# Optimization experiments

Measured on AMD Instinct MI355X. Metric: run time of the kernel, lower is better.

## Reference

```python
import jax, jax.numpy as jnp
import numpy as np

EMBED = 1024
HEADS = 16
HEAD_DIM = EMBED // HEADS
NEG = -1e20


def setup_inputs() -> dict:
    key = jax.random.key(0)
    k1, k2, k3, k4, k5, k6 = jax.random.split(key, 6)
    N, S = 2, 2048
    values = jax.random.normal(k1, (N, S, EMBED), dtype=jnp.float32)
    keys = jax.random.normal(k2, (N, S, EMBED), dtype=jnp.float32)
    query = jax.random.normal(k3, (N, S, EMBED), dtype=jnp.float32)
    mask = jax.random.randint(k4, (N, 1, S, S), 0, 2, dtype=jnp.int32)
    # fc_out: Linear(embed, embed) with bias; torch layout W [out, in]
    W_fc = jax.random.normal(k5, (EMBED, EMBED), dtype=jnp.float32) * (1.0 / np.sqrt(EMBED))
    b_fc = jax.random.normal(k6, (EMBED,), dtype=jnp.float32) * 0.01
    return {"values": values, "keys": keys, "query": query, "mask": mask,
            "W_fc": W_fc, "b_fc": b_fc}


def reference(values, keys, query, mask, W_fc, b_fc):
    N, Q, E = query.shape
    K = keys.shape[1]
    H, D = HEADS, HEAD_DIM
    v = values.reshape(N, K, H, D)
    k = keys.reshape(N, K, H, D)
    q = query.reshape(N, Q, H, D)
    # energy: [N, H, Q, K]
    energy = jnp.einsum('nqhd,nkhd->nhqk', q, k)
    energy = jnp.where(mask == 0, NEG, energy)
    # NOTE: original scales by sqrt(embed_size), not sqrt(head_dim)
    attn = jax.nn.softmax(energy / jnp.sqrt(jnp.float32(E)), axis=3)
    out = jnp.einsum('nhqk,nkhd->nqhd', attn, v).reshape(N, Q, H * D)
    return out @ W_fc.T + b_fc
```

## Files before the change

kernel.cpp:

```cpp
#include <hip/hip_runtime.h>
#include <cmath>

#define S_LEN 2048
#define EMB   1024
#define NHEAD 16
#define DHEAD 64
#define PIT   72

typedef __attribute__((ext_vector_type(8))) short bf16x8;
typedef __attribute__((ext_vector_type(4))) float f32x4;

__device__ __forceinline__ unsigned short f2bf(float f){
    union { float f; unsigned u; } v; v.f = f;
    unsigned r = v.u + 0x7fffu + ((v.u >> 16) & 1u);
    return (unsigned short)(r >> 16);
}

__device__ __forceinline__ unsigned pk2bf(float a, float b){
#if __has_builtin(__builtin_amdgcn_cvt_pk_bf16_f32)
    typedef __attribute__((ext_vector_type(2))) __bf16 bf2;
    bf2 r = __builtin_amdgcn_cvt_pk_bf16_f32(a, b);
    return *(unsigned*)&r;
#else
    return (unsigned)f2bf(a) | ((unsigned)f2bf(b) << 16);
#endif
}

__device__ __forceinline__ float fast_exp2(float x){
#if __has_builtin(__builtin_amdgcn_exp2f)
    return __builtin_amdgcn_exp2f(x);
#else
    return exp2f(x);
#endif
}

__device__ __forceinline__ float fast_rcp(float x){
#if __has_builtin(__builtin_amdgcn_rcpf)
    return __builtin_amdgcn_rcpf(x);
#else
    return 1.0f / x;
#endif
}

__global__ void prep_all(const float* __restrict__ q, const float* __restrict__ k,
                         const float* __restrict__ v, const int* __restrict__ mask,
                         const float* __restrict__ W,
                         unsigned short* __restrict__ Qb, unsigned short* __restrict__ Kb,
                         unsigned short* __restrict__ Vt, unsigned short* __restrict__ Wb,
                         unsigned* __restrict__ Mb){
    __shared__ unsigned short tile[64*68];
    const int b = blockIdx.x, tid = threadIdx.x;
    if (b < 4096){
        const float SC = 0.045084220027780106f;
        int base = (b*256 + tid) * 4;
        int e = base & (EMB - 1);
        int s = (base >> 10) & (S_LEN - 1);
        int n = base >> 21;
        int h = e >> 6, d = e & 63;
        int dst = ((n*NHEAD + h)*S_LEN + s)*DHEAD + d;
        float4 qv = *(const float4*)(q + base);
        float4 kv = *(const float4*)(k + base);
        uint2 qp, kp;
        qp.x = pk2bf(qv.x*SC, qv.y*SC);
        qp.y = pk2bf(qv.z*SC, qv.w*SC);
        kp.x = pk2bf(kv.x, kv.y);
        kp.y = pk2bf(kv.z, kv.w);
        *(uint2*)(Qb + dst) = qp;
        *(uint2*)(Kb + dst) = kp;
    } else if (b < 5120){
        int idx = b - 4096;
        int st = idx & 31, h = (idx >> 5) & 15, n = idx >> 9;
        int sbase = st * 64;
#pragma unroll
        for (int i = 0; i < 4; i++){
            int c = tid + i*256;
            int srow = c >> 4, c4 = (c & 15) * 4;
            float4 x = *(const float4*)(v + (n*S_LEN + sbase + srow)*EMB + h*DHEAD + c4);
            uint2 p;
            p.x = pk2bf(x.x, x.y);
            p.y = pk2bf(x.z, x.w);
            *(uint2*)&tile[srow*68 + c4] = p;
        }
        __syncthreads();
#pragma unroll
        for (int i = 0; i < 2; i++){
            int c = tid + i*256;
            int d = c >> 3, s8 = (c & 7) * 8;
            unsigned u0 = (unsigned)tile[(s8+0)*68 + d] | ((unsigned)tile[(s8+1)*68 + d] << 16);
            unsigned u1 = (unsigned)tile[(s8+2)*68 + d] | ((unsigned)tile[(s8+3)*68 + d] << 16);
            unsigned u2 = (unsigned)tile[(s8+4)*68 + d] | ((unsigned)tile[(s8+5)*68 + d] << 16);
            unsigned u3 = (unsigned)tile[(s8+6)*68 + d] | ((unsigned)tile[(s8+7)*68 + d] << 16);
            uint4 pk; pk.x = u0; pk.y = u1; pk.z = u2; pk.w = u3;
            *(uint4*)(Vt + ((n*NHEAD + h)*DHEAD + d)*S_LEN + sbase + s8) = pk;
        }
    } else if (b < 6144){
        int base = ((b - 5120)*256 + tid) * 4;
        float4 x = *(const float4*)(W + base);
        uint2 p;
        p.x = pk2bf(x.x, x.y);
        p.y = pk2bf(x.z, x.w);
        *(uint2*)(Wb + base) = p;
    } else {
        int u = (b - 6144)*256 + tid;
        const int4* m4 = (const int4*)mask + (size_t)u*8;
        unsigned w = 0;
#pragma unroll
        for (int i = 0; i < 8; i++){
            int4 m = m4[i];
            unsigned nib = (m.x ? 1u : 0u) | (m.y ? 2u : 0u) | (m.z ? 4u : 0u) | (m.w ? 8u : 0u);
            w |= nib << (i*4);
        }
        Mb[u] = w;
    }
}

__global__ __launch_bounds__(256, 4) void flash_attn(
    const unsigned short* __restrict__ Qb, const unsigned short* __restrict__ Kb,
    const unsigned short* __restrict__ Vt, const unsigned* __restrict__ Mb,
    float* __restrict__ Op, float* __restrict__ Lp){
    __shared__ unsigned short Kt[64*PIT];
    __shared__ unsigned short Vl[64*PIT];
    __shared__ unsigned short Pt[4][32*PIT];
    __shared__ uint2 mlut[16];

    const int tid = threadIdx.x;
    if (tid < 16){
        uint2 e;
        e.x = ((tid & 1) ? 0xFFFFu : 0u) | ((tid & 2) ? 0xFFFF0000u : 0u);
        e.y = ((tid & 4) ? 0xFFFFu : 0u) | ((tid & 8) ? 0xFFFF0000u : 0u);
        mlut[tid] = e;
    }

    const int flat = blockIdx.x + (blockIdx.y << 4) + (blockIdx.z << 9);
    const int xcd = flat & 7, idx = flat >> 3;
    const int qt = idx & 15;
    const int sl = xcd + ((idx >> 4) << 3);
    const int h = sl & 15, split = (sl >> 4) & 1, n = sl >> 5;

    const int wave = tid >> 6, lane = tid & 63, il = lane & 15, quad = lane >> 4;
    const int qbase = qt*128 + wave*32;
    const int kbase = split*1024;

    const unsigned short* Qh = Qb + (n*NHEAD + h)*S_LEN*DHEAD;
    const unsigned short* Kh = Kb + (n*NHEAD + h)*S_LEN*DHEAD + kbase*DHEAD;
    const unsigned short* Vh = Vt + (n*NHEAD + h)*DHEAD*S_LEN + kbase;
    const unsigned* mr0 = Mb + (size_t)(n*S_LEN + qbase + il)*(S_LEN/32) + (kbase >> 5);
    const unsigned* mr1 = mr0 + 16*(S_LEN/32);
    Op += (size_t)split * (2*S_LEN*EMB);
    Lp += split * (2*NHEAD*S_LEN);

    const int srow = tid >> 3, scol = (tid & 7)*8;

    bf16x8 Qf[2][2];
#pragma unroll
    for (int rt = 0; rt < 2; rt++)
#pragma unroll
        for (int ks = 0; ks < 2; ks++)
            Qf[rt][ks] = *(const bf16x8*)(Qh + (qbase + rt*16 + il)*DHEAD + ks*32 + quad*8);

    f32x4 acc[2][4], accL[2];
#pragma unroll
    for (int rt = 0; rt < 2; rt++){
        accL[rt] = (f32x4){0.f,0.f,0.f,0.f};
#pragma unroll
        for (int j = 0; j < 4; j++) acc[rt][j] = (f32x4){0.f,0.f,0.f,0.f};
    }
    const short onev = 0x3F80;
    const bf16x8 onesb = {onev,onev,onev,onev,onev,onev,onev,onev};

    unsigned short* Pw = Pt[wave];
    const int q4 = quad*4;

    uint4 kpre0 = *(const uint4*)(Kh + srow*DHEAD + scol);
    uint4 kpre1 = *(const uint4*)(Kh + (srow + 32)*DHEAD + scol);
    uint4 vpre0 = *(const uint4*)(Vh + srow*S_LEN + scol);
    uint4 vpre1 = *(const uint4*)(Vh + (srow + 32)*S_LEN + scol);

    for (int kb = 0; kb < 1024; kb += 64){
        *(uint4*)&Kt[srow*PIT + scol]        = kpre0;
        *(uint4*)&Kt[(srow + 32)*PIT + scol] = kpre1;
        *(uint4*)&Vl[srow*PIT + scol]        = vpre0;
        *(uint4*)&Vl[(srow + 32)*PIT + scol] = vpre1;
        __syncthreads();
        uint2 w0 = *(const uint2*)(mr0 + (kb >> 5));
        uint2 w1 = *(const uint2*)(mr1 + (kb >> 5));
        if (kb + 64 < 1024){
            kpre0 = *(const uint4*)(Kh + (kb + 64 + srow)*DHEAD + scol);
            kpre1 = *(const uint4*)(Kh + (kb + 64 + srow + 32)*DHEAD + scol);
            vpre0 = *(const uint4*)(Vh + srow*S_LEN + kb + 64 + scol);
            vpre1 = *(const uint4*)(Vh + (srow + 32)*S_LEN + kb + 64 + scol);
        }

        f32x4 e[2][4];
#pragma unroll
        for (int t = 0; t < 4; t++){
            bf16x8 kf0 = *(const bf16x8*)(&Kt[(t*16 + il)*PIT + quad*8]);
            bf16x8 kf1 = *(const bf16x8*)(&Kt[(t*16 + il)*PIT + 32 + quad*8]);
#pragma unroll
            for (int rt = 0; rt < 2; rt++){
                f32x4 z = (f32x4){0.f,0.f,0.f,0.f};
                z        = __builtin_amdgcn_mfma_f32_16x16x32_bf16(kf0, Qf[rt][0], z, 0, 0, 0);
                e[rt][t] = __builtin_amdgcn_mfma_f32_16x16x32_bf16(kf1, Qf[rt][1], z, 0, 0, 0);
            }
        }
#pragma unroll
        for (int rt = 0; rt < 2; rt++){
            const uint2 w = rt ? w1 : w0;
            unsigned s0 = w.x >> q4, s1 = w.y >> q4;
            unsigned s0h = s0 >> 16, s1h = s1 >> 16;
#pragma unroll
            for (int t = 0; t < 4; t++){
                unsigned s = (t == 0) ? s0 : (t == 1) ? s0h : (t == 2) ? s1 : s1h;
                uint2 mw = mlut[s & 0xFu];
                float p0 = fast_exp2(e[rt][t][0]);
                float p1 = fast_exp2(e[rt][t][1]);
                float p2 = fast_exp2(e[rt][t][2]);
                float p3 = fast_exp2(e[rt][t][3]);
                uint2 pk;
                pk.x = pk2bf(p0, p1) & mw.x;
                pk.y = pk2bf(p2, p3) & mw.y;
                *(uint2*)&Pw[(rt*16 + il)*PIT + t*16 + quad*4] = pk;
            }
        }
#pragma unroll
        for (int kk = 0; kk < 2; kk++){
            bf16x8 Pa[2];
#pragma unroll
            for (int rt = 0; rt < 2; rt++){
                Pa[rt] = *(const bf16x8*)(&Pw[(rt*16 + il)*PIT + kk*32 + quad*8]);
                accL[rt] = __builtin_amdgcn_mfma_f32_16x16x32_bf16(Pa[rt], onesb, accL[rt], 0, 0, 0);
            }
#pragma unroll
            for (int dt = 0; dt < 4; dt++){
                bf16x8 Vf = *(const bf16x8*)(&Vl[(dt*16 + il)*PIT + kk*32 + quad*8]);
#pragma unroll
                for (int rt = 0; rt < 2; rt++)
                    acc[rt][dt] = __builtin_amdgcn_mfma_f32_16x16x32_bf16(Pa[rt], Vf, acc[rt][dt], 0, 0, 0);
            }
        }
        __syncthreads();
    }

#pragma unroll
    for (int rt = 0; rt < 2; rt++){
#pragma unroll
        for (int dt = 0; dt < 4; dt++)
#pragma unroll
            for (int r = 0; r < 4; r++){
                size_t row = (size_t)(n*S_LEN + qbase + rt*16 + quad*4 + r);
                Op[row*EMB + h*DHEAD + dt*16 + il] = acc[rt][dt][r];
            }
        if (il == 0){
#pragma unroll
            for (int r = 0; r < 4; r++)
                Lp[(n*NHEAD + h)*S_LEN + qbase + rt*16 + quad*4 + r] = accL[rt][r];
        }
    }
}

__global__ __launch_bounds__(256, 2) void gemm_norm(
    const float* __restrict__ Op0, const float* __restrict__ Op1,
    const float* __restrict__ Lp0, const float* __restrict__ Lp1,
    const unsigned short* __restrict__ W, const float* __restrict__ bias,
    float* __restrict__ out){
    __shared__ unsigned short At[128*PIT];
    __shared__ unsigned short Wt[64*PIT];
    const int flat = blockIdx.x + (blockIdx.y << 4);
    const int xcd = flat & 7, idx = flat >> 3;
    const int nb = idx & 15, mb = xcd*4 + (idx >> 4);
    const int tid = threadIdx.x;
    const int wave = tid >> 6, lane = tid & 63, il = lane & 15, quad = lane >> 4;
    const int wm = wave & 1, wn = wave >> 1;
    const int mbase = mb*128, nbase = nb*64;
    const int arow = tid >> 3, acol = (tid & 7)*8;
    const int n_blk = mbase >> 11, qoff = (mbase & (S_LEN-1));
    const float* La = Lp0 + n_blk*NHEAD*S_LEN + qoff;
    const float* Lb = Lp1 + n_blk*NHEAD*S_LEN + qoff;

    f32x4 acc[4][2];
#pragma unroll
    for (int i = 0; i < 4; i++)
#pragma unroll
        for (int j = 0; j < 2; j++) acc[i][j] = (f32x4){0.f,0.f,0.f,0.f};

    float4 apre[4][2], bpre[4][2]; float lpa[4], lpb[4]; uint4 wpre[2];
#pragma unroll
    for (int j = 0; j < 4; j++){
        size_t off = (size_t)(mbase + arow + j*32)*EMB + acol;
        apre[j][0] = *(const float4*)(Op0 + off);
        apre[j][1] = *(const float4*)(Op0 + off + 4);
        bpre[j][0] = *(const float4*)(Op1 + off);
        bpre[j][1] = *(const float4*)(Op1 + off + 4);
        lpa[j] = La[arow + j*32];
        lpb[j] = Lb[arow + j*32];
    }
#pragma unroll
    for (int j = 0; j < 2; j++)
        wpre[j] = *(const uint4*)(W + (size_t)(nbase + arow + j*32)*EMB + acol);

    for (int kb = 0; kb < EMB; kb += 64){
#pragma unroll
        for (int j = 0; j < 4; j++){
            float inv = fast_rcp(lpa[j] + lpb[j]);
            uint4 pk;
            pk.x = pk2bf((apre[j][0].x + bpre[j][0].x)*inv, (apre[j][0].y + bpre[j][0].y)*inv);
            pk.y = pk2bf((apre[j][0].z + bpre[j][0].z)*inv, (apre[j][0].w + bpre[j][0].w)*inv);
            pk.z = pk2bf((apre[j][1].x + bpre[j][1].x)*inv, (apre[j][1].y + bpre[j][1].y)*inv);
            pk.w = pk2bf((apre[j][1].z + bpre[j][1].z)*inv, (apre[j][1].w + bpre[j][1].w)*inv);
            *(uint4*)&At[(arow + j*32)*PIT + acol] = pk;
        }
#pragma unroll
        for (int j = 0; j < 2; j++)
            *(uint4*)&Wt[(arow + j*32)*PIT + acol] = wpre[j];
        __syncthreads();
        if (kb + 64 < EMB){
            int h = (kb + 64) >> 6;
#pragma unroll
            for (int j = 0; j < 4; j++){
                size_t off = (size_t)(mbase + arow + j*32)*EMB + kb + 64 + acol;
                apre[j][0] = *(const float4*)(Op0 + off);
                apre[j][1] = *(const float4*)(Op0 + off + 4);
                bpre[j][0] = *(const float4*)(Op1 + off);
                bpre[j][1] = *(const float4*)(Op1 + off + 4);
                lpa[j] = La[h*S_LEN + arow + j*32];
                lpb[j] = Lb[h*S_LEN + arow + j*32];
            }
#pragma unroll
            for (int j = 0; j < 2; j++)
                wpre[j] = *(const uint4*)(W + (size_t)(nbase + arow + j*32)*EMB + kb + 64 + acol);
        }
#pragma unroll
        for (int ks = 0; ks < 2; ks++){
            bf16x8 Af[4], Wf[2];
#pragma unroll
            for (int mt = 0; mt < 4; mt++)
                Af[mt] = *(const bf16x8*)(&At[(wm*64 + mt*16 + il)*PIT + ks*32 + quad*8]);
#pragma unroll
            for (int nt = 0; nt < 2; nt++)
                Wf[nt] = *(const bf16x8*)(&Wt[(wn*32 + nt*16 + il)*PIT + ks*32 + quad*8]);
#pragma unroll
            for (int mt = 0; mt < 4; mt++)
#pragma unroll
                for (int nt = 0; nt < 2; nt++)
                    acc[mt][nt] = __builtin_amdgcn_mfma_f32_16x16x32_bf16(Af[mt], Wf[nt], acc[mt][nt], 0, 0, 0);
        }
        __syncthreads();
    }
    float bb[2];
#pragma unroll
    for (int nt = 0; nt < 2; nt++) bb[nt] = bias[nbase + wn*32 + nt*16 + il];
#pragma unroll
    for (int mt = 0; mt < 4; mt++)
#pragma unroll
        for (int nt = 0; nt < 2; nt++)
#pragma unroll
            for (int r = 0; r < 4; r++){
                int row = mbase + wm*64 + mt*16 + quad*4 + r;
                int col = nbase + wn*32 + nt*16 + il;
                out[(size_t)row*EMB + col] = acc[mt][nt][r] + bb[nt];
            }
}

extern "C" void kernel_launch(void* const* d_in, const int* in_sizes, int n_in,
                              void* d_out, int out_size, void* d_ws, size_t ws_size,
                              hipStream_t stream){
    const float* values = (const float*)d_in[0];
    const float* keys   = (const float*)d_in[1];
    const float* query  = (const float*)d_in[2];
    const int*   mask   = (const int*)d_in[3];
    const float* W_fc   = (const float*)d_in[4];
    const float* b_fc   = (const float*)d_in[5];
    float* out = (float*)d_out;

    char* ws = (char*)d_ws;
    unsigned short* Qb  = (unsigned short*)(ws);
    unsigned short* Kb  = (unsigned short*)(ws + (8ull  << 20));
    unsigned short* Vtb = (unsigned short*)(ws + (16ull << 20));
    unsigned short* Wb  = (unsigned short*)(ws + (24ull << 20));
    unsigned*       Mb  = (unsigned*)      (ws + (26ull << 20));
    float*          Op0 = (float*)         (ws + (27ull << 20));
    float*          Op1 = (float*)         (ws + (43ull << 20));
    float*          Lp0 = (float*)         (ws + (59ull << 20));
    float*          Lp1 = (float*)         (ws + (59ull << 20) + (256ull << 10));

    prep_all  <<<7168, 256, 0, stream>>>(query, keys, values, mask, W_fc,
                                         Qb, Kb, Vtb, Wb, Mb);
    flash_attn<<<dim3(16, 32, 2), 256, 0, stream>>>(Qb, Kb, Vtb, Mb, Op0, Lp0);
    gemm_norm <<<dim3(16, 32), 256, 0, stream>>>(Op0, Op1, Lp0, Lp1, Wb, b_fc, out);
}
```

Baseline: 236.8 us.

## Keep P in registers via 16x16x16 MFMA and shrink output GEMM tiles

In the attention kernel the softmax probabilities no longer round-trip through shared memory. The QK^T MFMA output layout already matches the A-operand layout of the 16x16x16 bf16 MFMA, so P is packed in registers and fed directly to the PV and row-sum MFMAs. This removes the per-wave P LDS buffer, its writes and reads, at the cost of twice as many smaller MFMA instructions. Separately, the projection GEMM uses 64x64 tiles instead of 128x64 with launch bounds for 4 blocks per CU and twice the grid, to improve occupancy and load balance at the expense of more W reloads.

```diff
diff --git a/kernel.cpp b/kernel.cpp
--- a/kernel.cpp
+++ b/kernel.cpp
@@ -8,7 +8,10 @@
 #define PIT   72
 
 typedef __attribute__((ext_vector_type(8))) short bf16x8;
+typedef __attribute__((ext_vector_type(4))) short bf16x4;
 typedef __attribute__((ext_vector_type(4))) float f32x4;
+
+#define MFMA16(a,b,c) __builtin_amdgcn_mfma_f32_16x16x16bf16_1k(a,b,c,0,0,0)
 
 __device__ __forceinline__ unsigned short f2bf(float f){
     union { float f; unsigned u; } v; v.f = f;
@@ -120,7 +123,6 @@
     float* __restrict__ Op, float* __restrict__ Lp){
     __shared__ unsigned short Kt[64*PIT];
     __shared__ unsigned short Vl[64*PIT];
-    __shared__ unsigned short Pt[4][32*PIT];
     __shared__ uint2 mlut[16];
 
     const int tid = threadIdx.x;
@@ -166,9 +168,8 @@
         for (int j = 0; j < 4; j++) acc[rt][j] = (f32x4){0.f,0.f,0.f,0.f};
     }
     const short onev = 0x3F80;
-    const bf16x8 onesb = {onev,onev,onev,onev,onev,onev,onev,onev};
-
-    unsigned short* Pw = Pt[wave];
+    const bf16x4 ones4 = {onev,onev,onev,onev};
+
     const int q4 = quad*4;
 
     uint4 kpre0 = *(const uint4*)(Kh + srow*DHEAD + scol);
@@ -203,6 +204,7 @@
                 e[rt][t] = __builtin_amdgcn_mfma_f32_16x16x32_bf16(kf1, Qf[rt][1], z, 0, 0, 0);
             }
         }
+        unsigned pw[2][4][2];
 #pragma unroll
         for (int rt = 0; rt < 2; rt++){
             const uint2 w = rt ? w1 : w0;
@@ -216,26 +218,25 @@
                 float p1 = fast_exp2(e[rt][t][1]);
                 float p2 = fast_exp2(e[rt][t][2]);
                 float p3 = fast_exp2(e[rt][t][3]);
-                uint2 pk;
-                pk.x = pk2bf(p0, p1) & mw.x;
-                pk.y = pk2bf(p2, p3) & mw.y;
-                *(uint2*)&Pw[(rt*16 + il)*PIT + t*16 + quad*4] = pk;
-            }
-        }
-#pragma unroll
-        for (int kk = 0; kk < 2; kk++){
-            bf16x8 Pa[2];
+                pw[rt][t][0] = pk2bf(p0, p1) & mw.x;
+                pw[rt][t][1] = pk2bf(p2, p3) & mw.y;
+            }
+        }
+#pragma unroll
+        for (int t = 0; t < 4; t++){
+            bf16x4 Pa[2];
 #pragma unroll
             for (int rt = 0; rt < 2; rt++){
-                Pa[rt] = *(const bf16x8*)(&Pw[(rt*16 + il)*PIT + kk*32 + quad*8]);
-                accL[rt] = __builtin_amdgcn_mfma_f32_16x16x32_bf16(Pa[rt], onesb, accL[rt], 0, 0, 0);
+                uint2 u; u.x = pw[rt][t][0]; u.y = pw[rt][t][1];
+                Pa[rt] = *(bf16x4*)&u;
+                accL[rt] = MFMA16(Pa[rt], ones4, accL[rt]);
             }
 #pragma unroll
             for (int dt = 0; dt < 4; dt++){
-                bf16x8 Vf = *(const bf16x8*)(&Vl[(dt*16 + il)*PIT + kk*32 + quad*8]);
+                bf16x4 Vf = *(const bf16x4*)(&Vl[(dt*16 + il)*PIT + t*16 + quad*4]);
 #pragma unroll
                 for (int rt = 0; rt < 2; rt++)
-                    acc[rt][dt] = __builtin_amdgcn_mfma_f32_16x16x32_bf16(Pa[rt], Vf, acc[rt][dt], 0, 0, 0);
+                    acc[rt][dt] = MFMA16(Pa[rt], Vf, acc[rt][dt]);
             }
         }
         __syncthreads();
@@ -244,12 +245,13 @@
 #pragma unroll
     for (int rt = 0; rt < 2; rt++){
 #pragma unroll
-        for (int dt = 0; dt < 4; dt++)
-#pragma unroll
-            for (int r = 0; r < 4; r++){
-                size_t row = (size_t)(n*S_LEN + qbase + rt*16 + quad*4 + r);
-                Op[row*EMB + h*DHEAD + dt*16 + il] = acc[rt][dt][r];
-            }
+        for (int r = 0; r < 4; r++){
+            size_t row = (size_t)(n*S_LEN + qbase + rt*16 + quad*4 + r);
+            float* dst = &Op[row*EMB + h*DHEAD + il];
+#pragma unroll
+            for (int dt = 0; dt < 4; dt++)
+                dst[dt*16] = acc[rt][dt][r];
+        }
         if (il == 0){
 #pragma unroll
             for (int r = 0; r < 4; r++)
@@ -258,88 +260,87 @@
     }
 }
 
-__global__ __launch_bounds__(256, 2) void gemm_norm(
+__global__ __launch_bounds__(256, 4) void gemm_norm(
     const float* __restrict__ Op0, const float* __restrict__ Op1,
     const float* __restrict__ Lp0, const float* __restrict__ Lp1,
     const unsigned short* __restrict__ W, const float* __restrict__ bias,
     float* __restrict__ out){
-    __shared__ unsigned short At[128*PIT];
+    __shared__ unsigned short At[64*PIT];
     __shared__ unsigned short Wt[64*PIT];
     const int flat = blockIdx.x + (blockIdx.y << 4);
     const int xcd = flat & 7, idx = flat >> 3;
-    const int nb = idx & 15, mb = xcd*4 + (idx >> 4);
+    const int nb = idx & 15, mb = xcd*8 + (idx >> 4);
     const int tid = threadIdx.x;
     const int wave = tid >> 6, lane = tid & 63, il = lane & 15, quad = lane >> 4;
     const int wm = wave & 1, wn = wave >> 1;
-    const int mbase = mb*128, nbase = nb*64;
-    const int arow = tid >> 3, acol = (tid & 7)*8;
+    const int mbase = mb*64, nbase = nb*64;
+    const int arow = tid >> 2, acol4 = (tid & 3)*16;
     const int n_blk = mbase >> 11, qoff = (mbase & (S_LEN-1));
-    const float* La = Lp0 + n_blk*NHEAD*S_LEN + qoff;
-    const float* Lb = Lp1 + n_blk*NHEAD*S_LEN + qoff;
-
-    f32x4 acc[4][2];
-#pragma unroll
-    for (int i = 0; i < 4; i++)
+    const float* La = Lp0 + n_blk*NHEAD*S_LEN + qoff + arow;
+    const float* Lb = Lp1 + n_blk*NHEAD*S_LEN + qoff + arow;
+
+    f32x4 acc[2][2];
+#pragma unroll
+    for (int i = 0; i < 2; i++)
 #pragma unroll
         for (int j = 0; j < 2; j++) acc[i][j] = (f32x4){0.f,0.f,0.f,0.f};
 
-    float4 apre[4][2], bpre[4][2]; float lpa[4], lpb[4]; uint4 wpre[2];
-#pragma unroll
-    for (int j = 0; j < 4; j++){
-        size_t off = (size_t)(mbase + arow + j*32)*EMB + acol;
-        apre[j][0] = *(const float4*)(Op0 + off);
-        apre[j][1] = *(const float4*)(Op0 + off + 4);
-        bpre[j][0] = *(const float4*)(Op1 + off);
-        bpre[j][1] = *(const float4*)(Op1 + off + 4);
-        lpa[j] = La[arow + j*32];
-        lpb[j] = Lb[arow + j*32];
-    }
+    float4 apre[4], bpre[4]; float lpa, lpb; uint4 wpre[2];
+    const size_t aoff = (size_t)(mbase + arow)*EMB + acol4;
+    const size_t woff = (size_t)(nbase + arow)*EMB + acol4;
+#pragma unroll
+    for (int i = 0; i < 4; i++){
+        apre[i] = *(const float4*)(Op0 + aoff + i*4);
+        bpre[i] = *(const float4*)(Op1 + aoff + i*4);
+    }
+    lpa = La[0];
+    lpb = Lb[0];
 #pragma unroll
     for (int j = 0; j < 2; j++)
-        wpre[j] = *(const uint4*)(W + (size_t)(nbase + arow + j*32)*EMB + acol);
+        wpre[j] = *(const uint4*)(W + woff + j*8);
 
     for (int kb = 0; kb < EMB; kb += 64){
-#pragma unroll
-        for (int j = 0; j < 4; j++){
-            float inv = fast_rcp(lpa[j] + lpb[j]);
-            uint4 pk;
-            pk.x = pk2bf((apre[j][0].x + bpre[j][0].x)*inv, (apre[j][0].y + bpre[j][0].y)*inv);
-            pk.y = pk2bf((apre[j][0].z + bpre[j][0].z)*inv, (apre[j][0].w + bpre[j][0].w)*inv);
-            pk.z = pk2bf((apre[j][1].x + bpre[j][1].x)*inv, (apre[j][1].y + bpre[j][1].y)*inv);
-            pk.w = pk2bf((apre[j][1].z + bpre[j][1].z)*inv, (apre[j][1].w + bpre[j][1].w)*inv);
-            *(uint4*)&At[(arow + j*32)*PIT + acol] = pk;
-        }
-#pragma unroll
-        for (int j = 0; j < 2; j++)
-            *(uint4*)&Wt[(arow + j*32)*PIT + acol] = wpre[j];
+        {
+            float inv = fast_rcp(lpa + lpb);
+            uint4 pk0, pk1;
+            pk0.x = pk2bf((apre[0].x + bpre[0].x)*inv, (apre[0].y + bpre[0].y)*inv);
+            pk0.y = pk2bf((apre[0].z + bpre[0].z)*inv, (apre[0].w + bpre[0].w)*inv);
+            pk0.z = pk2bf((apre[1].x + bpre[1].x)*inv, (apre[1].y + bpre[1].y)*inv);
+            pk0.w = pk2bf((apre[1].z + bpre[1].z)*inv, (apre[1].w + bpre[1].w)*inv);
+            pk1.x = pk2bf((apre[2].x + bpre[2].x)*inv, (apre[2].y + bpre[2].y)*inv);
+            pk1.y = pk2bf((apre[2].z + bpre[2].z)*inv, (apre[2].w + bpre[2].w)*inv);
+            pk1.z = pk2bf((apre[3].x + bpre[3].x)*inv, (apre[3].y + bpre[3].y)*inv);
+            pk1.w = pk2bf((apre[3].z + bpre[3].z)*inv, (apre[3].w + bpre[3].w)*inv);
+            *(uint4*)&At[arow*PIT + acol4]     = pk0;
+            *(uint4*)&At[arow*PIT + acol4 + 8] = pk1;
+            *(uint4*)&Wt[arow*PIT + acol4]     = wpre[0];
+            *(uint4*)&Wt[arow*PIT + acol4 + 8] = wpre[1];
+        }
         __syncthreads();
         if (kb + 64 < EMB){
-            int h = (kb + 64) >> 6;
-#pragma unroll
-            for (int j = 0; j < 4; j++){
-                size_t off = (size_t)(mbase + arow + j*32)*EMB + kb + 64 + acol;
-                apre[j][0] = *(const float4*)(Op0 + off);
-                apre[j][1] = *(const float4*)(Op0 + off + 4);
-                bpre[j][0] = *(const float4*)(Op1 + off);
-                bpre[j][1] = *(const float4*)(Op1 + off + 4);
-                lpa[j] = La[h*S_LEN + arow + j*32];
-                lpb[j] = Lb[h*S_LEN + arow + j*32];
-            }
+            int hh = (kb + 64) >> 6;
+#pragma unroll
+            for (int i = 0; i < 4; i++){
+                apre[i] = *(const float4*)(Op0 + aoff + kb + 64 + i*4);
+                bpre[i] = *(const float4*)(Op1 + aoff + kb + 64 + i*4);
+            }
+            lpa = La[hh*S_LEN];
+            lpb = Lb[hh*S_LEN];
 #pragma unroll
             for (int j = 0; j < 2; j++)
-                wpre[j] = *(const uint4*)(W + (size_t)(nbase + arow + j*32)*EMB + kb + 64 + acol);
+                wpre[j] = *(const uint4*)(W + woff + kb + 64 + j*8);
         }
 #pragma unroll
         for (int ks = 0; ks < 2; ks++){
-            bf16x8 Af[4], Wf[2];
-#pragma unroll
-            for (int mt = 0; mt < 4; mt++)
-                Af[mt] = *(const bf16x8*)(&At[(wm*64 + mt*16 + il)*PIT + ks*32 + quad*8]);
+            bf16x8 Af[2], Wf[2];
+#pragma unroll
+            for (int mt = 0; mt < 2; mt++)
+                Af[mt] = *(const bf16x8*)(&At[(wm*32 + mt*16 + il)*PIT + ks*32 + quad*8]);
 #pragma unroll
             for (int nt = 0; nt < 2; nt++)
                 Wf[nt] = *(const bf16x8*)(&Wt[(wn*32 + nt*16 + il)*PIT + ks*32 + quad*8]);
 #pragma unroll
-            for (int mt = 0; mt < 4; mt++)
+            for (int mt = 0; mt < 2; mt++)
 #pragma unroll
                 for (int nt = 0; nt < 2; nt++)
                     acc[mt][nt] = __builtin_amdgcn_mfma_f32_16x16x32_bf16(Af[mt], Wf[nt], acc[mt][nt], 0, 0, 0);
@@ -350,15 +351,15 @@
 #pragma unroll
     for (int nt = 0; nt < 2; nt++) bb[nt] = bias[nbase + wn*32 + nt*16 + il];
 #pragma unroll
-    for (int mt = 0; mt < 4; mt++)
-#pragma unroll
-        for (int nt = 0; nt < 2; nt++)
-#pragma unroll
-            for (int r = 0; r < 4; r++){
-                int row = mbase + wm*64 + mt*16 + quad*4 + r;
-                int col = nbase + wn*32 + nt*16 + il;
-                out[(size_t)row*EMB + col] = acc[mt][nt][r] + bb[nt];
-            }
+    for (int mt = 0; mt < 2; mt++)
+#pragma unroll
+        for (int r = 0; r < 4; r++){
+            int row = mbase + wm*32 + mt*16 + quad*4 + r;
+            float* dst = &out[(size_t)row*EMB + nbase + wn*32 + il];
+#pragma unroll
+            for (int nt = 0; nt < 2; nt++)
+                dst[nt*16] = acc[mt][nt][r] + bb[nt];
+        }
 }
 
 extern "C" void kernel_launch(void* const* d_in, const int* in_sizes, int n_in,
@@ -386,5 +387,5 @@
     prep_all  <<<7168, 256, 0, stream>>>(query, keys, values, mask, W_fc,
                                          Qb, Kb, Vtb, Wb, Mb);
     flash_attn<<<dim3(16, 32, 2), 256, 0, stream>>>(Qb, Kb, Vtb, Mb, Op0, Lp0);
-    gemm_norm <<<dim3(16, 32), 256, 0, stream>>>(Op0, Op1, Lp0, Lp1, Wb, b_fc, out);
-}
+    gemm_norm <<<dim3(16, 64), 256, 0, stream>>>(Op0, Op1, Lp0, Lp1, Wb, b_fc, out);
+}
```

Result: slower. 249.9 us (+5.6%).
